# Kernel optimization log

Hardware: AMD Instinct MI355X
Metric: run time of the kernel (lower is better)

Reference implementation:

```python
import jax, jax.numpy as jnp
import numpy as np

N = 10000   # nodes
E = 160000  # edges (before self-loops)
IN = 77     # input feature dim
H = 4       # heads (layers 1,2)
C = 128     # per-head out channels


def setup_inputs() -> dict:
    key = jax.random.key(0)
    ks = jax.random.split(key, 16)
    p = lambda k, shape: (jax.random.normal(k, shape, jnp.float32) * 0.1)
    z = lambda n: jnp.zeros((n,), jnp.float32)
    return {
        "x": jax.random.normal(ks[0], (N, IN), jnp.float32),
        "edge_index": jax.random.randint(ks[1], (2, E), 0, N),
        # layer 1: 77 -> H*C
        "Wl1": p(ks[2], (H * C, IN)), "bl1": z(H * C),
        "Wr1": p(ks[3], (H * C, IN)), "br1": z(H * C),
        "att1": p(ks[4], (H, C)), "b1": z(H * C),
        # layer 2: H*C -> H*C
        "Wl2": p(ks[5], (H * C, H * C)), "bl2": z(H * C),
        "Wr2": p(ks[6], (H * C, H * C)), "br2": z(H * C),
        "att2": p(ks[7], (H, C)), "b2": z(H * C),
        # layer 3: H*C -> C (1 head)
        "Wl3": p(ks[8], (C, H * C)), "bl3": z(C),
        "Wr3": p(ks[9], (C, H * C)), "br3": z(C),
        "att3": p(ks[10], (1, C)), "b3": z(C),
    }


def _gatv2_layer(x, src, dst, Wl, bl, Wr, br, att, bias, heads, outc):
    """PyG GATv2Conv (eval mode, self-loops already in src/dst, concat=True)."""
    n = x.shape[0]
    xl = (x @ Wl.T + bl).reshape(n, heads, outc)  # source transform
    xr = (x @ Wr.T + br).reshape(n, heads, outc)  # target transform
    # edge-wise score: a^T LeakyReLU(xl[src] + xr[dst])
    e = jax.nn.leaky_relu(xl[src] + xr[dst], negative_slope=0.2)  # [E,H,C]
    logits = jnp.einsum('ehc,hc->eh', e, att)                      # [E,H]
    # segment softmax over edges grouped by destination node
    m = jax.lax.stop_gradient(jax.ops.segment_max(logits, dst, num_segments=n))
    ev = jnp.exp(logits - m[dst])
    denom = jax.ops.segment_sum(ev, dst, num_segments=n)
    alpha = ev / (denom[dst] + 1e-16)                              # [E,H]
    # scatter-add weighted messages
    out = jax.ops.segment_sum(xl[src] * alpha[:, :, None], dst, num_segments=n)
    return out.reshape(n, heads * outc) + bias


def reference(x, edge_index, Wl1, bl1, Wr1, br1, att1, b1,
              Wl2, bl2, Wr2, br2, att2, b2,
              Wl3, bl3, Wr3, br3, att3, b3):
    n = x.shape[0]
    loop = jnp.arange(n)
    src = jnp.concatenate([edge_index[0], loop])  # add self-loops (PyG default)
    dst = jnp.concatenate([edge_index[1], loop])
    h = jax.nn.elu(_gatv2_layer(x, src, dst, Wl1, bl1, Wr1, br1, att1, b1, H, C))
    h = jax.nn.elu(_gatv2_layer(h, src, dst, Wl2, bl2, Wr2, br2, att2, b2, H, C))
    return _gatv2_layer(h, src, dst, Wl3, bl3, Wr3, br3, att3, b3, 1, C)
```

## Files before the change

### kernel.cpp

```cpp
#include <hip/hip_runtime.h>
#include <hip/hip_bf16.h>
#include <math.h>

typedef __attribute__((ext_vector_type(8))) short short8;
typedef __attribute__((ext_vector_type(4))) float f32x4;
typedef __attribute__((ext_vector_type(2))) float f32x2;

__device__ __forceinline__ float bf2f(unsigned short u) {
  union { unsigned int i; float f; } x; x.i = ((unsigned int)u) << 16; return x.f;
}

__device__ __forceinline__ void load_lds16(const void* g, void* l) {
  __builtin_amdgcn_global_load_lds(
      (const __attribute__((address_space(1))) unsigned int*)g,
      (__attribute__((address_space(3))) unsigned int*)l, 16, 0, 0);
}

__global__ __launch_bounds__(256) void gemm_mfma(
    const __hip_bfloat16* __restrict__ A, const __hip_bfloat16* __restrict__ B,
    const float* __restrict__ bl, const float* __restrict__ br, int halfN,
    __hip_bfloat16* __restrict__ out, int M, int K, int Nout) {
  __shared__ __hip_bfloat16 As[128 * 32];
  __shared__ __hip_bfloat16 Bs[128 * 32];
  int t = threadIdx.x;
  int w = t >> 6, l = t & 63;
  int lr = l & 15, lh = l >> 4;
  int wr = w >> 1, wc = w & 1;
  int m0 = blockIdx.y * 128, n0 = blockIdx.x * 128;
  f32x4 acc[4][4] = {};
  int nk = K >> 5;
  for (int ks = 0; ks < nk; ++ks) {
    int k0 = ks << 5;
#pragma unroll
    for (int p = 0; p < 2; ++p) {
      int c = p * 256 + t;
      int row = c >> 2, sub = c & 3;
      int gm = m0 + row; if (gm >= M) gm = M - 1;
      const __hip_bfloat16* gsrc = A + (size_t)gm * K + k0 + sub * 8;
      char* ldst = (char*)As + (size_t)(p * 256 + w * 64) * 16;
      load_lds16(gsrc, ldst);
    }
#pragma unroll
    for (int p = 0; p < 2; ++p) {
      int c = p * 256 + t;
      int row = c >> 2, sub = c & 3;
      const __hip_bfloat16* gsrc = B + (size_t)(n0 + row) * K + k0 + sub * 8;
      char* ldst = (char*)Bs + (size_t)(p * 256 + w * 64) * 16;
      load_lds16(gsrc, ldst);
    }
    __syncthreads();
    short8 af[4], bf[4];
#pragma unroll
    for (int mt = 0; mt < 4; ++mt)
      af[mt] = *(const short8*)(As + (size_t)(wr * 64 + mt * 16 + lr) * 32 + lh * 8);
#pragma unroll
    for (int nt = 0; nt < 4; ++nt)
      bf[nt] = *(const short8*)(Bs + (size_t)(wc * 64 + nt * 16 + lr) * 32 + lh * 8);
#pragma unroll
    for (int mt = 0; mt < 4; ++mt)
#pragma unroll
      for (int nt = 0; nt < 4; ++nt)
        acc[mt][nt] = __builtin_amdgcn_mfma_f32_16x16x32_bf16(af[mt], bf[nt], acc[mt][nt], 0, 0, 0);
    __syncthreads();
  }
#pragma unroll
  for (int mt = 0; mt < 4; ++mt) {
#pragma unroll
    for (int r = 0; r < 4; ++r) {
      int gm = m0 + wr * 64 + mt * 16 + lh * 4 + r;
      if (gm >= M) continue;
#pragma unroll
      for (int nt = 0; nt < 4; ++nt) {
        int gn = n0 + wc * 64 + nt * 16 + lr;
        float bv = (gn < halfN) ? bl[gn] : br[gn - halfN];
        out[(size_t)gm * Nout + gn] = __float2bfloat16(acc[mt][nt][r] + bv);
      }
    }
  }
}

struct CastSeg { const float* src; __hip_bfloat16* dst; int rows, K, Kp, row0, start; };
struct CastArgs { CastSeg s[7]; int total; };

__global__ __launch_bounds__(256) void k_cast_all(CastArgs A) {
  int stride = gridDim.x * blockDim.x;
  for (int i = blockIdx.x * blockDim.x + threadIdx.x; i < A.total; i += stride) {
    int si = 0;
#pragma unroll
    for (int j = 1; j < 7; j++) if (i >= A.s[j].start) si = j;
    CastSeg sg = A.s[si];
    int li = i - sg.start;
    int r = li / sg.Kp, k = li - r * sg.Kp;
    float v = (k < sg.K) ? sg.src[(size_t)r * sg.K + k] : 0.f;
    sg.dst[(size_t)(sg.row0 + r) * sg.Kp + k] = __float2bfloat16(v);
  }
}

__global__ void k_hist(const int* __restrict__ ei, int E, int N, int* __restrict__ deg) {
  int e = blockIdx.x * blockDim.x + threadIdx.x;
  int ET = E + N;
  if (e >= ET) return;
  int d = (e < E) ? ei[E + e] : (e - E);
  atomicAdd(&deg[d], 1);
}

__global__ __launch_bounds__(256) void k_scan_one(const int* __restrict__ deg, int N,
                                                  int* __restrict__ rp, int* __restrict__ cursor) {
  __shared__ int part[256];
  int t = threadIdx.x;
  int chunk = (N + 255) / 256;
  int lo = t * chunk;
  int hi = lo + chunk; if (hi > N) hi = N;
  int s = 0;
  for (int i = lo; i < hi; ++i) s += deg[i];
  part[t] = s;
  __syncthreads();
  for (int off = 1; off < 256; off <<= 1) {
    int x = (t >= off) ? part[t - off] : 0;
    __syncthreads();
    part[t] += x;
    __syncthreads();
  }
  int run = (t == 0) ? 0 : part[t - 1];
  for (int i = lo; i < hi; ++i) {
    rp[i] = run;
    cursor[i] = run;
    run += deg[i];
  }
  if (t == 255) rp[N] = run;
}

__global__ void k_scatter(const int* __restrict__ ei, int E, int N,
                          int* __restrict__ cursor, int* __restrict__ srcs) {
  int e = blockIdx.x * blockDim.x + threadIdx.x;
  int ET = E + N;
  if (e >= ET) return;
  int s = (e < E) ? ei[e] : (e - E);
  int d = (e < E) ? ei[E + e] : (e - E);
  int pos = atomicAdd(&cursor[d], 1);
  srcs[pos] = s;
}

template <int CPL> struct VecSel;
template <> struct VecSel<8> { using T = short8; };
template <> struct VecSel<2> { using T = unsigned int; };

template <int HC, int Hn, bool ELU, typename OutT>
__global__ __launch_bounds__(256) void k_edge_fused(
    const __hip_bfloat16* __restrict__ xl, const __hip_bfloat16* __restrict__ xr, int LD,
    const int* __restrict__ rp, const int* __restrict__ srcs,
    const float* __restrict__ att, const float* __restrict__ bias,
    int N, OutT* __restrict__ out) {
  const int CPL = HC / 64;
  using VecT = typename VecSel<CPL>::T;
  int lane = threadIdx.x & 63;
  int n = (blockIdx.x * blockDim.x + threadIdx.x) >> 6;
  if (n >= N) return;
  float a[CPL], xrv[CPL];
#pragma unroll
  for (int c = 0; c < CPL; c++) a[c] = att[lane * CPL + c];
  if constexpr (CPL == 8) {
    short8 v = *(const short8*)(xr + (size_t)n * LD + lane * 8);
#pragma unroll
    for (int c = 0; c < 8; c++) xrv[c] = bf2f((unsigned short)v[c]);
  } else {
    unsigned int v = *(const unsigned int*)(xr + (size_t)n * LD + lane * 2);
    xrv[0] = bf2f((unsigned short)(v & 0xffff));
    xrv[1] = bf2f((unsigned short)(v >> 16));
  }
  int s0 = rp[n], s1 = rp[n + 1];
  float m = -INFINITY, sum = 0.f;
  float acc[CPL] = {};

  auto loadrow = [&](int s) -> VecT {
    return *(const VecT*)(xl + (size_t)s * LD + lane * CPL);
  };
  auto proc = [&](VecT v) {
    float xv[CPL];
    if constexpr (CPL == 8) {
#pragma unroll
      for (int c = 0; c < 8; c++) xv[c] = bf2f((unsigned short)v[c]);
    } else {
      xv[0] = bf2f((unsigned short)(v & 0xffff));
      xv[1] = bf2f((unsigned short)(v >> 16));
    }
    float p = 0.f;
#pragma unroll
    for (int c = 0; c < CPL; c++) {
      float t2 = xv[c] + xrv[c];
      t2 = t2 > 0.f ? t2 : 0.2f * t2;
      p = fmaf(t2, a[c], p);
    }
    const int RO = (Hn == 4) ? 8 : 32;
#pragma unroll
    for (int off = 1; off <= RO; off <<= 1) p += __shfl_xor(p, off, 64);
    if (__any(p > m + 8.f)) {
      float mn = fmaxf(m, p);
      float corr = __expf(m - mn);
      float wgt = __expf(p - mn);
      sum = sum * corr + wgt;
#pragma unroll
      for (int c = 0; c < CPL; c++) acc[c] = fmaf(acc[c], corr, wgt * xv[c]);
      m = mn;
    } else {
      float wgt = __expf(p - m);
      sum += wgt;
#pragma unroll
      for (int c = 0; c < CPL; c++) acc[c] = fmaf(wgt, xv[c], acc[c]);
    }
  };

  VecT b0, b1;
  b0 = loadrow(srcs[s0]);
  if (s0 + 1 < s1) b1 = loadrow(srcs[s0 + 1]);
  int i = s0;
  for (; i + 1 < s1; i += 2) {
    VecT n0v, n1v;
    bool pf = (i + 2 < s1);
    if (pf) {
      int j0 = srcs[i + 2];
      int j1 = (i + 3 < s1) ? srcs[i + 3] : j0;
      n0v = loadrow(j0);
      n1v = loadrow(j1);
    }
    proc(b0);
    proc(b1);
    if (pf) { b0 = n0v; b1 = n1v; }
  }
  if (i < s1) proc(b0);

  float inv = 1.f / (sum + 1e-16f);
#pragma unroll
  for (int c = 0; c < CPL; c++) {
    float r = acc[c] * inv + bias[lane * CPL + c];
    if (ELU) r = r > 0.f ? r : expm1f(r);
    acc[c] = r;
  }
  if constexpr (sizeof(OutT) == 2) {
    short8 o;
#pragma unroll
    for (int c = 0; c < CPL; c++) {
      __hip_bfloat16 bv = __float2bfloat16(acc[c]);
      o[c] = __builtin_bit_cast(short, bv);
    }
    *(short8*)((__hip_bfloat16*)out + (size_t)n * HC + lane * CPL) = o;
  } else {
    f32x2 o; o.x = acc[0]; o.y = acc[1];
    *(f32x2*)((float*)out + (size_t)n * HC + lane * 2) = o;
  }
}

extern "C" void kernel_launch(void* const* d_in, const int* in_sizes, int n_in,
                              void* d_out, int out_size, void* d_ws, size_t ws_size,
                              hipStream_t stream) {
  const int IN = 77, Kp1 = 96, Hh = 4, Cc = 128, HC = Hh * Cc;
  const int N = in_sizes[0] / IN;
  const int E = in_sizes[1] / 2;
  const int ET = E + N;

  const float* x   = (const float*)d_in[0];
  const int*   ei  = (const int*)d_in[1];
  const float* Wl1 = (const float*)d_in[2];  const float* bl1 = (const float*)d_in[3];
  const float* Wr1 = (const float*)d_in[4];  const float* br1 = (const float*)d_in[5];
  const float* att1= (const float*)d_in[6];  const float* b1  = (const float*)d_in[7];
  const float* Wl2 = (const float*)d_in[8];  const float* bl2 = (const float*)d_in[9];
  const float* Wr2 = (const float*)d_in[10]; const float* br2 = (const float*)d_in[11];
  const float* att2= (const float*)d_in[12]; const float* b2  = (const float*)d_in[13];
  const float* Wl3 = (const float*)d_in[14]; const float* bl3 = (const float*)d_in[15];
  const float* Wr3 = (const float*)d_in[16]; const float* br3 = (const float*)d_in[17];
  const float* att3= (const float*)d_in[18]; const float* b3  = (const float*)d_in[19];
  float* out = (float*)d_out;

  char* w = (char*)d_ws;
  size_t off = 0;
  auto alloc = [&](size_t bytes) -> void* {
    void* p = w + off;
    off += (bytes + 255) & ~(size_t)255;
    return p;
  };
  __hip_bfloat16* xlr = (__hip_bfloat16*)alloc((size_t)N * 2 * HC * 2);
  __hip_bfloat16* hb  = (__hip_bfloat16*)alloc((size_t)N * HC * 2);
  __hip_bfloat16* Wc1 = (__hip_bfloat16*)alloc((size_t)2 * HC * Kp1 * 2);
  __hip_bfloat16* Wc2 = (__hip_bfloat16*)alloc((size_t)2 * HC * HC * 2);
  __hip_bfloat16* Wc3 = (__hip_bfloat16*)alloc((size_t)2 * Cc * HC * 2);
  int*   deg    = (int*)alloc((size_t)N * 4);
  int*   rp     = (int*)alloc((size_t)(N + 1) * 4);
  int*   cursor = (int*)alloc((size_t)N * 4);
  int*   srcs   = (int*)alloc((size_t)ET * 4);

  CastArgs CA;
  int cum = 0;
  auto seg = [&](int idx, const float* src, __hip_bfloat16* dst, int rows, int K, int Kp, int row0) {
    CA.s[idx] = {src, dst, rows, K, Kp, row0, cum};
    cum += rows * Kp;
  };
  seg(0, Wl1, Wc1, HC, IN, Kp1, 0);
  seg(1, Wr1, Wc1, HC, IN, Kp1, HC);
  seg(2, Wl2, Wc2, HC, HC, HC, 0);
  seg(3, Wr2, Wc2, HC, HC, HC, HC);
  seg(4, Wl3, Wc3, Cc, HC, HC, 0);
  seg(5, Wr3, Wc3, Cc, HC, HC, Cc);
  seg(6, x,   hb,  N,  IN, Kp1, 0);
  CA.total = cum;
  k_cast_all<<<1024, 256, 0, stream>>>(CA);

  hipMemsetAsync(deg, 0, (size_t)N * 4, stream);
  int tb = 256;
  k_hist<<<(ET + tb - 1) / tb, tb, 0, stream>>>(ei, E, N, deg);
  k_scan_one<<<1, 256, 0, stream>>>(deg, N, rp, cursor);
  k_scatter<<<(ET + tb - 1) / tb, tb, 0, stream>>>(ei, E, N, cursor, srcs);

  int nodeBlocks = (N + 3) / 4;
  int mb = (N + 127) / 128;

  {
    dim3 g(2 * HC / 128, mb);
    gemm_mfma<<<g, 256, 0, stream>>>(hb, Wc1, bl1, br1, HC, xlr, N, Kp1, 2 * HC);
    k_edge_fused<512, 4, true, __hip_bfloat16><<<nodeBlocks, 256, 0, stream>>>(
        xlr, xlr + HC, 2 * HC, rp, srcs, att1, b1, N, hb);
  }
  {
    dim3 g(2 * HC / 128, mb);
    gemm_mfma<<<g, 256, 0, stream>>>(hb, Wc2, bl2, br2, HC, xlr, N, HC, 2 * HC);
    k_edge_fused<512, 4, true, __hip_bfloat16><<<nodeBlocks, 256, 0, stream>>>(
        xlr, xlr + HC, 2 * HC, rp, srcs, att2, b2, N, hb);
  }
  {
    dim3 g(2 * Cc / 128, mb);
    gemm_mfma<<<g, 256, 0, stream>>>(hb, Wc3, bl3, br3, Cc, xlr, N, HC, 2 * Cc);
    k_edge_fused<128, 1, false, float><<<nodeBlocks, 256, 0, stream>>>(
        xlr, xlr + Cc, 2 * Cc, rp, srcs, att3, b3, N, out);
  }
}
```

Baseline: 225.0 us.

## Split each node's edge list across two wavefronts and merge softmax in LDS

Result: no change. 226.4 us (+0.6%).

```diff
diff --git a/kernel.cpp b/kernel.cpp
--- a/kernel.cpp
+++ b/kernel.cpp
@@ -145,108 +145,137 @@
 template <> struct VecSel<8> { using T = short8; };
 template <> struct VecSel<2> { using T = unsigned int; };
 
-template <int HC, int Hn, bool ELU, typename OutT>
-__global__ __launch_bounds__(256) void k_edge_fused(
-    const __hip_bfloat16* __restrict__ xl, const __hip_bfloat16* __restrict__ xr, int LD,
+template <int HC, int Hn, int LDc, bool ELU, typename OutT>
+__global__ __launch_bounds__(512) void k_edge_fused(
+    const __hip_bfloat16* __restrict__ xl, const __hip_bfloat16* __restrict__ xr,
     const int* __restrict__ rp, const int* __restrict__ srcs,
     const float* __restrict__ att, const float* __restrict__ bias,
     int N, OutT* __restrict__ out) {
   const int CPL = HC / 64;
   using VecT = typename VecSel<CPL>::T;
+  __shared__ float lds_acc[4][HC];
+  __shared__ float lds_m[4][64];
+  __shared__ float lds_s[4][64];
   int lane = threadIdx.x & 63;
-  int n = (blockIdx.x * blockDim.x + threadIdx.x) >> 6;
-  if (n >= N) return;
+  int wv = threadIdx.x >> 6;
+  int slot = wv >> 1, half = wv & 1;
+  int n = blockIdx.x * 4 + slot;
+  bool active = n < N;
+
   float a[CPL], xrv[CPL];
-#pragma unroll
-  for (int c = 0; c < CPL; c++) a[c] = att[lane * CPL + c];
-  if constexpr (CPL == 8) {
-    short8 v = *(const short8*)(xr + (size_t)n * LD + lane * 8);
-#pragma unroll
-    for (int c = 0; c < 8; c++) xrv[c] = bf2f((unsigned short)v[c]);
-  } else {
-    unsigned int v = *(const unsigned int*)(xr + (size_t)n * LD + lane * 2);
-    xrv[0] = bf2f((unsigned short)(v & 0xffff));
-    xrv[1] = bf2f((unsigned short)(v >> 16));
-  }
-  int s0 = rp[n], s1 = rp[n + 1];
   float m = -INFINITY, sum = 0.f;
   float acc[CPL] = {};
 
-  auto loadrow = [&](int s) -> VecT {
-    return *(const VecT*)(xl + (size_t)s * LD + lane * CPL);
-  };
-  auto proc = [&](VecT v) {
-    float xv[CPL];
+  if (active) {
+#pragma unroll
+    for (int c = 0; c < CPL; c++) a[c] = att[lane * CPL + c];
     if constexpr (CPL == 8) {
-#pragma unroll
-      for (int c = 0; c < 8; c++) xv[c] = bf2f((unsigned short)v[c]);
+      short8 v = *(const short8*)(xr + (size_t)n * LDc + lane * 8);
+#pragma unroll
+      for (int c = 0; c < 8; c++) xrv[c] = bf2f((unsigned short)v[c]);
     } else {
-      xv[0] = bf2f((unsigned short)(v & 0xffff));
-      xv[1] = bf2f((unsigned short)(v >> 16));
-    }
-    float p = 0.f;
+      unsigned int v = *(const unsigned int*)(xr + (size_t)n * LDc + lane * 2);
+      xrv[0] = bf2f((unsigned short)(v & 0xffff));
+      xrv[1] = bf2f((unsigned short)(v >> 16));
+    }
+    int s0 = rp[n], s1 = rp[n + 1];
+    int mid = s0 + ((s1 - s0 + 1) >> 1);
+    int lo = half ? mid : s0;
+    int hi = half ? s1 : mid;
+
+    auto loadrow = [&](int s) -> VecT {
+      return *(const VecT*)(xl + (size_t)s * LDc + lane * CPL);
+    };
+    auto proc = [&](VecT v) {
+      float xv[CPL];
+      if constexpr (CPL == 8) {
+#pragma unroll
+        for (int c = 0; c < 8; c++) xv[c] = bf2f((unsigned short)v[c]);
+      } else {
+        xv[0] = bf2f((unsigned short)(v & 0xffff));
+        xv[1] = bf2f((unsigned short)(v >> 16));
+      }
+      float p = 0.f;
+#pragma unroll
+      for (int c = 0; c < CPL; c++) {
+        float t2 = xv[c] + xrv[c];
+        t2 = t2 > 0.f ? t2 : 0.2f * t2;
+        p = fmaf(t2, a[c], p);
+      }
+      const int RO = (Hn == 4) ? 8 : 32;
+#pragma unroll
+      for (int off = 1; off <= RO; off <<= 1) p += __shfl_xor(p, off, 64);
+      if (__any(p > m + 8.f)) {
+        float mn = fmaxf(m, p);
+        float corr = __expf(m - mn);
+        float wgt = __expf(p - mn);
+        sum = sum * corr + wgt;
+#pragma unroll
+        for (int c = 0; c < CPL; c++) acc[c] = fmaf(acc[c], corr, wgt * xv[c]);
+        m = mn;
+      } else {
+        float wgt = __expf(p - m);
+        sum += wgt;
+#pragma unroll
+        for (int c = 0; c < CPL; c++) acc[c] = fmaf(wgt, xv[c], acc[c]);
+      }
+    };
+
+    if (lo < hi) {
+      VecT b0, b1;
+      b0 = loadrow(srcs[lo]);
+      if (lo + 1 < hi) b1 = loadrow(srcs[lo + 1]);
+      int i = lo;
+      for (; i + 1 < hi; i += 2) {
+        VecT n0v, n1v;
+        bool pf = (i + 2 < hi);
+        if (pf) {
+          int j0 = srcs[i + 2];
+          int j1 = (i + 3 < hi) ? srcs[i + 3] : j0;
+          n0v = loadrow(j0);
+          n1v = loadrow(j1);
+        }
+        proc(b0);
+        proc(b1);
+        if (pf) { b0 = n0v; b1 = n1v; }
+      }
+      if (i < hi) proc(b0);
+    }
+  }
+
+  if (half) {
+    lds_m[slot][lane] = m;
+    lds_s[slot][lane] = sum;
+#pragma unroll
+    for (int c = 0; c < CPL; c++) lds_acc[slot][lane * CPL + c] = acc[c];
+  }
+  __syncthreads();
+  if (!half && active) {
+    float mB = lds_m[slot][lane];
+    float sB = lds_s[slot][lane];
+    float M = fmaxf(m, mB);
+    float cA = __expf(m - M);
+    float cB = __expf(mB - M);
+    float s = sum * cA + sB * cB;
+    float inv = 1.f / (s + 1e-16f);
 #pragma unroll
     for (int c = 0; c < CPL; c++) {
-      float t2 = xv[c] + xrv[c];
-      t2 = t2 > 0.f ? t2 : 0.2f * t2;
-      p = fmaf(t2, a[c], p);
-    }
-    const int RO = (Hn == 4) ? 8 : 32;
-#pragma unroll
-    for (int off = 1; off <= RO; off <<= 1) p += __shfl_xor(p, off, 64);
-    if (__any(p > m + 8.f)) {
-      float mn = fmaxf(m, p);
-      float corr = __expf(m - mn);
-      float wgt = __expf(p - mn);
-      sum = sum * corr + wgt;
-#pragma unroll
-      for (int c = 0; c < CPL; c++) acc[c] = fmaf(acc[c], corr, wgt * xv[c]);
-      m = mn;
+      float r = (acc[c] * cA + lds_acc[slot][lane * CPL + c] * cB) * inv + bias[lane * CPL + c];
+      if (ELU) r = r > 0.f ? r : expm1f(r);
+      acc[c] = r;
+    }
+    if constexpr (sizeof(OutT) == 2) {
+      short8 o;
+#pragma unroll
+      for (int c = 0; c < CPL; c++) {
+        __hip_bfloat16 bv = __float2bfloat16(acc[c]);
+        o[c] = __builtin_bit_cast(short, bv);
+      }
+      *(short8*)((__hip_bfloat16*)out + (size_t)n * HC + lane * CPL) = o;
     } else {
-      float wgt = __expf(p - m);
-      sum += wgt;
-#pragma unroll
-      for (int c = 0; c < CPL; c++) acc[c] = fmaf(wgt, xv[c], acc[c]);
-    }
-  };
-
-  VecT b0, b1;
-  b0 = loadrow(srcs[s0]);
-  if (s0 + 1 < s1) b1 = loadrow(srcs[s0 + 1]);
-  int i = s0;
-  for (; i + 1 < s1; i += 2) {
-    VecT n0v, n1v;
-    bool pf = (i + 2 < s1);
-    if (pf) {
-      int j0 = srcs[i + 2];
-      int j1 = (i + 3 < s1) ? srcs[i + 3] : j0;
-      n0v = loadrow(j0);
-      n1v = loadrow(j1);
-    }
-    proc(b0);
-    proc(b1);
-    if (pf) { b0 = n0v; b1 = n1v; }
-  }
-  if (i < s1) proc(b0);
-
-  float inv = 1.f / (sum + 1e-16f);
-#pragma unroll
-  for (int c = 0; c < CPL; c++) {
-    float r = acc[c] * inv + bias[lane * CPL + c];
-    if (ELU) r = r > 0.f ? r : expm1f(r);
-    acc[c] = r;
-  }
-  if constexpr (sizeof(OutT) == 2) {
-    short8 o;
-#pragma unroll
-    for (int c = 0; c < CPL; c++) {
-      __hip_bfloat16 bv = __float2bfloat16(acc[c]);
-      o[c] = __builtin_bit_cast(short, bv);
-    }
-    *(short8*)((__hip_bfloat16*)out + (size_t)n * HC + lane * CPL) = o;
-  } else {
-    f32x2 o; o.x = acc[0]; o.y = acc[1];
-    *(f32x2*)((float*)out + (size_t)n * HC + lane * 2) = o;
+      f32x2 o; o.x = acc[0]; o.y = acc[1];
+      *(f32x2*)((float*)out + (size_t)n * HC + lane * 2) = o;
+    }
   }
 }
 
@@ -316,19 +345,19 @@
   {
     dim3 g(2 * HC / 128, mb);
     gemm_mfma<<<g, 256, 0, stream>>>(hb, Wc1, bl1, br1, HC, xlr, N, Kp1, 2 * HC);
-    k_edge_fused<512, 4, true, __hip_bfloat16><<<nodeBlocks, 256, 0, stream>>>(
-        xlr, xlr + HC, 2 * HC, rp, srcs, att1, b1, N, hb);
+    k_edge_fused<512, 4, 1024, true, __hip_bfloat16><<<nodeBlocks, 512, 0, stream>>>(
+        xlr, xlr + HC, rp, srcs, att1, b1, N, hb);
   }
   {
     dim3 g(2 * HC / 128, mb);
     gemm_mfma<<<g, 256, 0, stream>>>(hb, Wc2, bl2, br2, HC, xlr, N, HC, 2 * HC);
-    k_edge_fused<512, 4, true, __hip_bfloat16><<<nodeBlocks, 256, 0, stream>>>(
-        xlr, xlr + HC, 2 * HC, rp, srcs, att2, b2, N, hb);
+    k_edge_fused<512, 4, 1024, true, __hip_bfloat16><<<nodeBlocks, 512, 0, stream>>>(
+        xlr, xlr + HC, rp, srcs, att2, b2, N, hb);
   }
   {
     dim3 g(2 * Cc / 128, mb);
     gemm_mfma<<<g, 256, 0, stream>>>(hb, Wc3, bl3, br3, Cc, xlr, N, HC, 2 * Cc);
-    k_edge_fused<128, 1, false, float><<<nodeBlocks, 256, 0, stream>>>(
-        xlr, xlr + Cc, 2 * Cc, rp, srcs, att3, b3, N, out);
-  }
-}
+    k_edge_fused<128, 1, 256, false, float><<<nodeBlocks, 512, 0, stream>>>(
+        xlr, xlr + Cc, rp, srcs, att3, b3, N, out);
+  }
+}
```

## Use four independent online-softmax streams with deeper row prefetch in edge kernel

Applied to the files above, without the earlier changes.

Result: slower. 355.4 us (+57.9%).

```diff
diff --git a/kernel.cpp b/kernel.cpp
--- a/kernel.cpp
+++ b/kernel.cpp
@@ -145,9 +145,9 @@
 template <> struct VecSel<8> { using T = short8; };
 template <> struct VecSel<2> { using T = unsigned int; };
 
-template <int HC, int Hn, bool ELU, typename OutT>
-__global__ __launch_bounds__(256) void k_edge_fused(
-    const __hip_bfloat16* __restrict__ xl, const __hip_bfloat16* __restrict__ xr, int LD,
+template <int HC, int Hn, int LDc, bool ELU, typename OutT>
+__global__ __launch_bounds__(256, 4) void k_edge_fused(
+    const __hip_bfloat16* __restrict__ xl, const __hip_bfloat16* __restrict__ xr,
     const int* __restrict__ rp, const int* __restrict__ srcs,
     const float* __restrict__ att, const float* __restrict__ bias,
     int N, OutT* __restrict__ out) {
@@ -156,26 +156,35 @@
   int lane = threadIdx.x & 63;
   int n = (blockIdx.x * blockDim.x + threadIdx.x) >> 6;
   if (n >= N) return;
+
   float a[CPL], xrv[CPL];
 #pragma unroll
   for (int c = 0; c < CPL; c++) a[c] = att[lane * CPL + c];
   if constexpr (CPL == 8) {
-    short8 v = *(const short8*)(xr + (size_t)n * LD + lane * 8);
+    short8 v = *(const short8*)(xr + (size_t)n * LDc + lane * 8);
 #pragma unroll
     for (int c = 0; c < 8; c++) xrv[c] = bf2f((unsigned short)v[c]);
   } else {
-    unsigned int v = *(const unsigned int*)(xr + (size_t)n * LD + lane * 2);
+    unsigned int v = *(const unsigned int*)(xr + (size_t)n * LDc + lane * 2);
     xrv[0] = bf2f((unsigned short)(v & 0xffff));
     xrv[1] = bf2f((unsigned short)(v >> 16));
   }
+
   int s0 = rp[n], s1 = rp[n + 1];
-  float m = -INFINITY, sum = 0.f;
-  float acc[CPL] = {};
+  int len = s1 - s0;
+  float m[4], sum[4];
+  float acc[4][CPL];
+#pragma unroll
+  for (int j = 0; j < 4; ++j) {
+    m[j] = -INFINITY; sum[j] = 0.f;
+#pragma unroll
+    for (int c = 0; c < CPL; ++c) acc[j][c] = 0.f;
+  }
 
   auto loadrow = [&](int s) -> VecT {
-    return *(const VecT*)(xl + (size_t)s * LD + lane * CPL);
+    return *(const VecT*)(xl + (size_t)s * LDc + lane * CPL);
   };
-  auto proc = [&](VecT v) {
+  auto proc = [&](int j, VecT v) {
     float xv[CPL];
     if constexpr (CPL == 8) {
 #pragma unroll
@@ -194,58 +203,69 @@
     const int RO = (Hn == 4) ? 8 : 32;
 #pragma unroll
     for (int off = 1; off <= RO; off <<= 1) p += __shfl_xor(p, off, 64);
-    if (__any(p > m + 8.f)) {
-      float mn = fmaxf(m, p);
-      float corr = __expf(m - mn);
+    if (__any(p > m[j] + 8.f)) {
+      float mn = fmaxf(m[j], p);
+      float corr = __expf(m[j] - mn);
       float wgt = __expf(p - mn);
-      sum = sum * corr + wgt;
-#pragma unroll
-      for (int c = 0; c < CPL; c++) acc[c] = fmaf(acc[c], corr, wgt * xv[c]);
-      m = mn;
+      sum[j] = sum[j] * corr + wgt;
+#pragma unroll
+      for (int c = 0; c < CPL; c++) acc[j][c] = fmaf(acc[j][c], corr, wgt * xv[c]);
+      m[j] = mn;
     } else {
-      float wgt = __expf(p - m);
-      sum += wgt;
-#pragma unroll
-      for (int c = 0; c < CPL; c++) acc[c] = fmaf(wgt, xv[c], acc[c]);
+      float wgt = __expf(p - m[j]);
+      sum[j] += wgt;
+#pragma unroll
+      for (int c = 0; c < CPL; c++) acc[j][c] = fmaf(wgt, xv[c], acc[j][c]);
     }
   };
 
-  VecT b0, b1;
-  b0 = loadrow(srcs[s0]);
-  if (s0 + 1 < s1) b1 = loadrow(srcs[s0 + 1]);
-  int i = s0;
-  for (; i + 1 < s1; i += 2) {
-    VecT n0v, n1v;
-    bool pf = (i + 2 < s1);
-    if (pf) {
-      int j0 = srcs[i + 2];
-      int j1 = (i + 3 < s1) ? srcs[i + 3] : j0;
-      n0v = loadrow(j0);
-      n1v = loadrow(j1);
-    }
-    proc(b0);
-    proc(b1);
-    if (pf) { b0 = n0v; b1 = n1v; }
-  }
-  if (i < s1) proc(b0);
-
-  float inv = 1.f / (sum + 1e-16f);
+  VecT buf[4];
+#pragma unroll
+  for (int j = 0; j < 4; ++j) if (j < len) buf[j] = loadrow(srcs[s0 + j]);
+  int i = 0;
+  for (; i + 4 <= len; i += 4) {
+    VecT nxt[4] = {buf[0], buf[1], buf[2], buf[3]};
+#pragma unroll
+    for (int j = 0; j < 4; ++j) {
+      int k = i + 4 + j;
+      if (k < len) nxt[j] = loadrow(srcs[s0 + k]);
+    }
+#pragma unroll
+    for (int j = 0; j < 4; ++j) proc(j, buf[j]);
+#pragma unroll
+    for (int j = 0; j < 4; ++j) buf[j] = nxt[j];
+  }
+#pragma unroll
+  for (int j = 0; j < 4; ++j) if (i + j < len) proc(j, buf[j]);
+
+#pragma unroll
+  for (int j = 1; j < 4; ++j) {
+    float M = fmaxf(m[0], m[j]);
+    float c0 = __expf(m[0] - M);
+    float cj = __expf(m[j] - M);
+    sum[0] = sum[0] * c0 + sum[j] * cj;
+#pragma unroll
+    for (int c = 0; c < CPL; ++c) acc[0][c] = acc[0][c] * c0 + acc[j][c] * cj;
+    m[0] = M;
+  }
+
+  float inv = 1.f / (sum[0] + 1e-16f);
 #pragma unroll
   for (int c = 0; c < CPL; c++) {
-    float r = acc[c] * inv + bias[lane * CPL + c];
+    float r = acc[0][c] * inv + bias[lane * CPL + c];
     if (ELU) r = r > 0.f ? r : expm1f(r);
-    acc[c] = r;
+    acc[0][c] = r;
   }
   if constexpr (sizeof(OutT) == 2) {
     short8 o;
 #pragma unroll
     for (int c = 0; c < CPL; c++) {
-      __hip_bfloat16 bv = __float2bfloat16(acc[c]);
+      __hip_bfloat16 bv = __float2bfloat16(acc[0][c]);
       o[c] = __builtin_bit_cast(short, bv);
     }
     *(short8*)((__hip_bfloat16*)out + (size_t)n * HC + lane * CPL) = o;
   } else {
-    f32x2 o; o.x = acc[0]; o.y = acc[1];
+    f32x2 o; o.x = acc[0][0]; o.y = acc[0][1];
     *(f32x2*)((float*)out + (size_t)n * HC + lane * 2) = o;
   }
 }
@@ -316,19 +336,19 @@
   {
     dim3 g(2 * HC / 128, mb);
     gemm_mfma<<<g, 256, 0, stream>>>(hb, Wc1, bl1, br1, HC, xlr, N, Kp1, 2 * HC);
-    k_edge_fused<512, 4, true, __hip_bfloat16><<<nodeBlocks, 256, 0, stream>>>(
-        xlr, xlr + HC, 2 * HC, rp, srcs, att1, b1, N, hb);
+    k_edge_fused<512, 4, 1024, true, __hip_bfloat16><<<nodeBlocks, 256, 0, stream>>>(
+        xlr, xlr + HC, rp, srcs, att1, b1, N, hb);
   }
   {
     dim3 g(2 * HC / 128, mb);
     gemm_mfma<<<g, 256, 0, stream>>>(hb, Wc2, bl2, br2, HC, xlr, N, HC, 2 * HC);
-    k_edge_fused<512, 4, true, __hip_bfloat16><<<nodeBlocks, 256, 0, stream>>>(
-        xlr, xlr + HC, 2 * HC, rp, srcs, att2, b2, N, hb);
+    k_edge_fused<512, 4, 1024, true, __hip_bfloat16><<<nodeBlocks, 256, 0, stream>>>(
+        xlr, xlr + HC, rp, srcs, att2, b2, N, hb);
   }
   {
     dim3 g(2 * Cc / 128, mb);
     gemm_mfma<<<g, 256, 0, stream>>>(hb, Wc3, bl3, br3, Cc, xlr, N, HC, 2 * Cc);
-    k_edge_fused<128, 1, false, float><<<nodeBlocks, 256, 0, stream>>>(
-        xlr, xlr + Cc, 2 * Cc, rp, srcs, att3, b3, N, out);
-  }
-}
+    k_edge_fused<128, 1, 256, false, float><<<nodeBlocks, 256, 0, stream>>>(
+        xlr, xlr + Cc, rp, srcs, att3, b3, N, out);
+  }
+}
```
